# Kernel optimization log

Hardware: AMD Instinct MI355X
Metric: run time of the kernel (lower is better)

## Reference

```python
import math
import jax, jax.numpy as jnp
import numpy as np

B, T, C = 4, 2048, 1024
H = 16
HS = C // H  # head_size = 64

def setup_inputs() -> dict:
    key = jax.random.key(0)
    k1, k2, k3 = jax.random.split(key, 3)
    x = jax.random.normal(k1, (B, T, C), dtype=jnp.float32)
    W_qkv = jax.random.normal(k2, (C, 3 * C), dtype=jnp.float32) * (1.0 / math.sqrt(C))
    W_proj = jax.random.normal(k3, (C, C), dtype=jnp.float32) * (1.0 / math.sqrt(C))
    b_proj = jnp.zeros((C,), dtype=jnp.float32)
    return {"x": x, "W_qkv": W_qkv, "W_proj": W_proj, "b_proj": b_proj}

def reference(x, W_qkv, W_proj, b_proj):
    Bx, Tx, Cx = x.shape
    qkv = x @ W_qkv  # [B,T,3C]
    q, k, v = jnp.split(qkv, 3, axis=-1)
    # [B,T,C] -> [B,H,T,HS]
    def heads(t):
        return t.reshape(Bx, Tx, H, HS).transpose(0, 2, 1, 3)
    q, k, v = heads(q), heads(k), heads(v)
    scores = jnp.einsum('bhqd,bhkd->bhqk', q, k) / math.sqrt(HS)
    causal = jnp.tril(jnp.ones((Tx, Tx), dtype=bool))
    scores = jnp.where(causal, scores, -jnp.inf)
    attn = jax.nn.softmax(scores, axis=-1)
    out = jnp.einsum('bhqk,bhkd->bhqd', attn, v)  # [B,H,T,HS]
    out = out.transpose(0, 2, 1, 3).reshape(Bx, Tx, Cx)
    return out @ W_proj + b_proj
```

## Files before the change

kernel.cpp:

```cpp
#include <hip/hip_runtime.h>
#include <hip/hip_bf16.h>
#include <cstdint>
#include <cstddef>

using bf16 = __hip_bfloat16;
typedef __attribute__((ext_vector_type(8))) short short8;
typedef __attribute__((ext_vector_type(4))) float floatx4;

#define B_ 4
#define T_ 2048
#define C_ 1024
#define H_ 16
#define HS_ 64
#define BT_ (B_*T_)
#define N3C (3*C_)

#define MFMA16(a,b,c) __builtin_amdgcn_mfma_f32_16x16x32_bf16((a),(b),(c),0,0,0)

#if __has_builtin(__builtin_amdgcn_exp2f)
#define EXP2(x) __builtin_amdgcn_exp2f(x)
#else
#define EXP2(x) exp2f(x)
#endif

static __device__ __forceinline__ void gld16(const bf16* g, bf16* l) {
  __builtin_amdgcn_global_load_lds(
      (const __attribute__((address_space(1))) unsigned int*)g,
      (__attribute__((address_space(3))) unsigned int*)l, 16, 0, 0);
}

__global__ void k_cast(const float* __restrict__ in, bf16* __restrict__ out, int n4) {
  int i = blockIdx.x * blockDim.x + threadIdx.x;
  if (i >= n4) return;
  float4 v = ((const float4*)in)[i];
  union { bf16 b[4]; uint2 u; } cvt;
  cvt.b[0] = __float2bfloat16(v.x);
  cvt.b[1] = __float2bfloat16(v.y);
  cvt.b[2] = __float2bfloat16(v.z);
  cvt.b[3] = __float2bfloat16(v.w);
  ((uint2*)out)[i] = cvt.u;
}

__global__ void k_tcast(const float* __restrict__ in, bf16* __restrict__ out, int K, int N) {
  __shared__ float tile[64][65];
  const int k0 = blockIdx.y * 64, n0 = blockIdx.x * 64;
  const int tid = threadIdx.x;
  const int r = tid >> 6, c = tid & 63;
  #pragma unroll
  for (int j = 0; j < 16; ++j)
    tile[r + j*4][c] = in[(size_t)(k0 + r + j*4) * N + n0 + c];
  __syncthreads();
  #pragma unroll
  for (int j = 0; j < 16; ++j) {
    int rr = r + j*4;
    out[(size_t)(n0 + rr) * K + k0 + c] = __float2bfloat16(tile[c][rr]);
  }
}

__global__ void k_vtrans(const bf16* __restrict__ Vb, bf16* __restrict__ Vt) {
  __shared__ unsigned short tile[64*65];
  const int tid = threadIdx.x;
  const int bh = blockIdx.y, t0 = blockIdx.x * 64;
  const unsigned int* src = (const unsigned int*)(Vb + (size_t)bh * T_ * HS_ + (size_t)t0 * HS_);
  #pragma unroll
  for (int it = 0; it < 8; ++it) {
    int id = it*256 + tid;
    int row = id >> 5, cd = id & 31;
    unsigned int v = src[row*32 + cd];
    tile[row*65 + cd*2]     = (unsigned short)(v & 0xffff);
    tile[row*65 + cd*2 + 1] = (unsigned short)(v >> 16);
  }
  __syncthreads();
  bf16* dst = Vt + (size_t)bh * HS_ * T_ + t0;
  #pragma unroll
  for (int it = 0; it < 8; ++it) {
    int o = it*256 + tid;
    int d = o >> 5, tp = o & 31;
    int k0p = tp + (tp & 16);
    unsigned int lo = tile[k0p*65 + d];
    unsigned int hi = tile[(k0p + 16)*65 + d];
    ((unsigned int*)(dst + (size_t)d * T_))[tp] = lo | (hi << 16);
  }
}

template<int MODE, int NB>
__global__ __launch_bounds__(256, 2)
void k_gemm(const bf16* __restrict__ A, const bf16* __restrict__ Bt,
            int N, int K,
            bf16* __restrict__ Qb, bf16* __restrict__ Kb, bf16* __restrict__ Vb,
            float* __restrict__ Out, const float* __restrict__ bias)
{
  __shared__ bf16 sA[2][128*32];
  __shared__ bf16 sB[2][128*32];
  const int tid  = threadIdx.x;
  const int lane = tid & 63, wave = tid >> 6;
  const int quad = lane >> 4, l16 = lane & 15;
  const int wm = wave >> 1, wn = wave & 1;

  const int g = blockIdx.x;
  const int xcd = g & 7;
  const int local = g >> 3;
  const int nb = local % NB;
  const int mb = (local / NB) * 8 + xcd;
  const int m0 = mb * 128, n0 = nb * 128;

  const int ra = tid >> 2;
  const int gc = (tid & 3) ^ ((ra >> 1) & 3);
  const bf16* aptr = A  + (size_t)(m0 + ra) * K + gc*8;
  const bf16* bptr = Bt + (size_t)(n0 + ra) * K + gc*8;
  const size_t rowjump = (size_t)64 * K;

  floatx4 acc[4][4] = {};
  const int KI = K >> 5;
  const int pc = quad ^ ((l16 >> 1) & 3);

  for (int i = 0; i <= KI; ++i) {
    __syncthreads();
    if (i < KI) {
      const int k0 = i << 5;
      bf16* sa = sA[i & 1]; bf16* sb = sB[i & 1];
      gld16(aptr + k0,           sa + tid*8);
      gld16(aptr + rowjump + k0, sa + 2048 + tid*8);
      gld16(bptr + k0,           sb + tid*8);
      gld16(bptr + rowjump + k0, sb + 2048 + tid*8);
    }
    if (i == 0) continue;
    const bf16* sa = sA[(i-1) & 1];
    const bf16* sb = sB[(i-1) & 1];
    short8 af[4], bfm[4];
    #pragma unroll
    for (int ii = 0; ii < 4; ++ii)
      af[ii] = *(const short8*)&sa[(wm*64 + ii*16 + l16) * 32 + pc*8];
    #pragma unroll
    for (int ii = 0; ii < 4; ++ii)
      bfm[ii] = *(const short8*)&sb[(wn*64 + ii*16 + l16) * 32 + pc*8];
    #pragma unroll
    for (int ii = 0; ii < 4; ++ii)
      #pragma unroll
      for (int j = 0; j < 4; ++j)
        acc[ii][j] = MFMA16(af[ii], bfm[j], acc[ii][j]);
  }

  #pragma unroll
  for (int i = 0; i < 4; ++i) {
    const int rowb = m0 + wm*64 + i*16 + quad*4;
    #pragma unroll
    for (int j = 0; j < 4; ++j) {
      const int col = n0 + wn*64 + j*16 + l16;
      #pragma unroll
      for (int r = 0; r < 4; ++r) {
        const float v = acc[i][j][r];
        const int rr = rowb + r;
        if (MODE == 0) {
          const int b = rr >> 11, t = rr & 2047;
          const int h = (col >> 6) & 15, d = col & 63;
          const size_t addr = (((size_t)(b*H_ + h) * T_ + t) << 6) + d;
          if (col < C_) {
            Qb[addr] = __float2bfloat16(v * 0.18033688f);
          } else if (col < 2*C_) {
            Kb[addr] = __float2bfloat16(v);
          } else {
            Vb[addr] = __float2bfloat16(v);
          }
        } else {
          Out[(size_t)rr * N + col] = v + bias[col];
        }
      }
    }
  }
}

__global__ __launch_bounds__(256, 2)
void k_attn(const bf16* __restrict__ Q, const bf16* __restrict__ K,
            const bf16* __restrict__ Vt, bf16* __restrict__ att)
{
  __shared__ bf16 kbuf[2][64*64];
  __shared__ bf16 vbuf[2][64*64];
  __shared__ bf16 pbuf[4][32*64];

  const int tid  = threadIdx.x;
  const int lane = tid & 63, wave = tid >> 6;
  const int quad = lane >> 4, l16 = lane & 15;
  const int x7 = l16 & 7;

  const int g  = blockIdx.x;
  const int bh = (g & 7) * 8 + (g >> 6);
  const int bx = (g >> 3) & 7;
  const int b = bh >> 4, h = bh & 15;

  const bf16* Qp = Q  + (size_t)bh * T_ * HS_;
  const bf16* Kp = K  + (size_t)bh * T_ * HS_;
  const bf16* Vp = Vt + (size_t)bh * HS_ * T_;

  const int qbase[2] = { (15-bx)*128 + wave*32, bx*128 + wave*32 };
  const int ntk0 = 32 - 2*bx;
  const int ntk1 = 2*bx + 2;

  short8 qf[2][2][2];
  #pragma unroll
  for (int t = 0; t < 2; ++t)
    #pragma unroll
    for (int mt = 0; mt < 2; ++mt)
      #pragma unroll
      for (int ss = 0; ss < 2; ++ss)
        qf[t][mt][ss] = *(const short8*)(Qp + (size_t)(qbase[t] + mt*16 + l16) * HS_ + ss*32 + quad*8);

  floatx4 o[2][2][4] = {};
  float lrow[2][2][4] = {};

  const bf16* kg[2]; const bf16* vg[2];
  int ldsoff[2];
  #pragma unroll
  for (int it = 0; it < 2; ++it) {
    const int c = it*256 + tid;
    const int row = c >> 3;
    const int col = (c & 7) ^ (row & 7);
    kg[it] = Kp + (size_t)row * HS_ + col*8;
    vg[it] = Vp + (size_t)row * T_ + col*8;
    ldsoff[it] = c*8;
  }

  bf16* pw = pbuf[wave];
  unsigned int* pw32 = (unsigned int*)pw;
  const int c0 = l16 >> 2;
  const int dwl = l16 & 3;

  for (int i = 0; i <= ntk0; ++i) {
    __syncthreads();
    if (i < ntk0) {
      const int stk0 = i * 64;
      bf16* kb = kbuf[i & 1];
      bf16* vb = vbuf[i & 1];
      #pragma unroll
      for (int it = 0; it < 2; ++it) {
        gld16(kg[it] + (size_t)stk0 * HS_, kb + ldsoff[it]);
        gld16(vg[it] + stk0,               vb + ldsoff[it]);
      }
    }
    if (i == 0) continue;
    const int tk  = i - 1;
    const int tk0 = tk * 64;
    const bf16* kb = kbuf[tk & 1];
    const bf16* vb = vbuf[tk & 1];

    #pragma unroll
    for (int t = 0; t < 2; ++t) {
      if (t == 1 && tk >= ntk1) break;
      if (tk0 > qbase[t] + 31) continue;

      floatx4 s[2][4] = {};
      #pragma unroll
      for (int nt = 0; nt < 4; ++nt) {
        const int key = nt*16 + l16;
        #pragma unroll
        for (int ss = 0; ss < 2; ++ss) {
          short8 kf = *(const short8*)&kb[(key*8 + ((ss*4+quad) ^ x7))*8];
          s[0][nt] = MFMA16(qf[t][0][ss], kf, s[0][nt]);
          s[1][nt] = MFMA16(qf[t][1][ss], kf, s[1][nt]);
        }
      }

      if (tk0 + 63 > qbase[t]) {
        #pragma unroll
        for (int mt = 0; mt < 2; ++mt)
          #pragma unroll
          for (int nt = 0; nt < 4; ++nt) {
            const int key = tk0 + nt*16 + l16;
            #pragma unroll
            for (int r = 0; r < 4; ++r) {
              const int qr = qbase[t] + mt*16 + quad*4 + r;
              if (key > qr) s[mt][nt][r] = -1e30f;
            }
          }
      }

      #pragma unroll
      for (int mt = 0; mt < 2; ++mt) {
        #pragma unroll
        for (int r = 0; r < 4; ++r) {
          const float p0 = EXP2(s[mt][0][r]), p1 = EXP2(s[mt][1][r]);
          const float p2 = EXP2(s[mt][2][r]), p3 = EXP2(s[mt][3][r]);
          lrow[t][mt][r] += (p0 + p1) + (p2 + p3);
          const int q = mt*16 + quad*4 + r;
          const unsigned w0 = __builtin_amdgcn_perm(__float_as_uint(p1), __float_as_uint(p0), 0x07060302u);
          const unsigned w1 = __builtin_amdgcn_perm(__float_as_uint(p3), __float_as_uint(p2), 0x07060302u);
          pw32[q*32 + (((c0 + q)     & 7) << 2) + dwl] = w0;
          pw32[q*32 + (((c0 + q + 4) & 7) << 2) + dwl] = w1;
        }
      }

      #pragma unroll
      for (int ss = 0; ss < 2; ++ss) {
        short8 pf0 = *(const short8*)&pw[l16*64      + ((4*ss + quad + l16) & 7)*8];
        short8 pf1 = *(const short8*)&pw[(16+l16)*64 + ((4*ss + quad + l16) & 7)*8];
        #pragma unroll
        for (int nd = 0; nd < 4; ++nd) {
          const int d = nd*16 + l16;
          short8 vf = *(const short8*)&vb[(d*8 + ((ss*4+quad) ^ x7))*8];
          o[t][0][nd] = MFMA16(pf0, vf, o[t][0][nd]);
          o[t][1][nd] = MFMA16(pf1, vf, o[t][1][nd]);
        }
      }
    }
  }

  #pragma unroll
  for (int t = 0; t < 2; ++t) {
    #pragma unroll
    for (int mt = 0; mt < 2; ++mt) {
      #pragma unroll
      for (int r = 0; r < 4; ++r) {
        float lsum = lrow[t][mt][r];
        lsum += __shfl_xor(lsum, 1);
        lsum += __shfl_xor(lsum, 2);
        lsum += __shfl_xor(lsum, 4);
        lsum += __shfl_xor(lsum, 8);
        const float inv = 1.0f / lsum;
        const int tt = qbase[t] + mt*16 + quad*4 + r;
        #pragma unroll
        for (int nd = 0; nd < 4; ++nd)
          att[(size_t)(b*T_ + tt) * C_ + h*64 + nd*16 + l16] =
              __float2bfloat16(o[t][mt][nd][r] * inv);
      }
    }
  }
}

extern "C" void kernel_launch(void* const* d_in, const int* in_sizes, int n_in,
                              void* d_out, int out_size, void* d_ws, size_t ws_size,
                              hipStream_t stream) {
  const float* x     = (const float*)d_in[0];
  const float* Wqkv  = (const float*)d_in[1];
  const float* Wproj = (const float*)d_in[2];
  const float* bproj = (const float*)d_in[3];
  float* out = (float*)d_out;

  char* ws = (char*)d_ws;
  bf16* xb     = (bf16*)(ws + 0);
  bf16* wqkvT  = (bf16*)(ws + 16777216);
  bf16* wprojT = (bf16*)(ws + 23068672);
  bf16* Qb     = (bf16*)(ws + 25165824);
  bf16* Kb     = (bf16*)(ws + 41943040);
  bf16* Vt     = (bf16*)(ws + 58720256);
  bf16* att    = (bf16*)(ws + 75497472);
  bf16* Vb     = att;

  k_cast<<<dim3(BT_*C_/4/256), 256, 0, stream>>>(x, xb, BT_*C_/4);
  k_tcast<<<dim3(N3C/64, C_/64), 256, 0, stream>>>(Wqkv, wqkvT, C_, N3C);
  k_tcast<<<dim3(C_/64, C_/64), 256, 0, stream>>>(Wproj, wprojT, C_, C_);
  k_gemm<0, 24><<<dim3(1536), 256, 0, stream>>>(
      xb, wqkvT, N3C, C_, Qb, Kb, Vb, nullptr, nullptr);
  k_vtrans<<<dim3(T_/64, B_*H_), 256, 0, stream>>>(Vb, Vt);
  k_attn<<<dim3(512), 256, 0, stream>>>(Qb, Kb, Vt, att);
  k_gemm<1, 8><<<dim3(512), 256, 0, stream>>>(
      att, wprojT, C_, C_, nullptr, nullptr, nullptr, out, bproj);
}
```

Baseline: 253.9 us.

## Fuse V transpose into QKV GEMM epilogue and merge cast kernels

The three input-cast kernels become a single prep launch, which saves launch overhead. The separate V transpose kernel is removed. Instead, blocks in the QKV GEMM that produce V columns stage the tile in shared memory and write V directly in the transposed, permuted layout that attention expects. This avoids one full write and read of the V tensor and one kernel launch. The cost is a bigger shared-memory footprint, about 33 KB, plus an extra barrier and LDS staging in those GEMM blocks.

```diff
diff --git a/kernel.cpp b/kernel.cpp
--- a/kernel.cpp
+++ b/kernel.cpp
@@ -29,22 +29,41 @@
       (__attribute__((address_space(3))) unsigned int*)l, 16, 0, 0);
 }
 
-__global__ void k_cast(const float* __restrict__ in, bf16* __restrict__ out, int n4) {
-  int i = blockIdx.x * blockDim.x + threadIdx.x;
-  if (i >= n4) return;
-  float4 v = ((const float4*)in)[i];
-  union { bf16 b[4]; uint2 u; } cvt;
-  cvt.b[0] = __float2bfloat16(v.x);
-  cvt.b[1] = __float2bfloat16(v.y);
-  cvt.b[2] = __float2bfloat16(v.z);
-  cvt.b[3] = __float2bfloat16(v.w);
-  ((uint2*)out)[i] = cvt.u;
-}
-
-__global__ void k_tcast(const float* __restrict__ in, bf16* __restrict__ out, int K, int N) {
+static __device__ __forceinline__ unsigned short f2bf_us(float x) {
+  bf16 b = __float2bfloat16(x);
+  return *(unsigned short*)&b;
+}
+
+__global__ __launch_bounds__(256)
+void k_prep(const float* __restrict__ x, bf16* __restrict__ xb,
+            const float* __restrict__ Wqkv, bf16* __restrict__ wqkvT,
+            const float* __restrict__ Wproj, bf16* __restrict__ wprojT)
+{
+  const int bid = blockIdx.x, tid = threadIdx.x;
   __shared__ float tile[64][65];
-  const int k0 = blockIdx.y * 64, n0 = blockIdx.x * 64;
-  const int tid = threadIdx.x;
+
+  if (bid < 8192) {
+    const int i = bid*256 + tid;
+    float4 v = ((const float4*)x)[i];
+    union { bf16 b[4]; uint2 u; } cvt;
+    cvt.b[0] = __float2bfloat16(v.x);
+    cvt.b[1] = __float2bfloat16(v.y);
+    cvt.b[2] = __float2bfloat16(v.z);
+    cvt.b[3] = __float2bfloat16(v.w);
+    ((uint2*)xb)[i] = cvt.u;
+    return;
+  }
+
+  const float* in; bf16* out; int N, n0, k0;
+  if (bid < 8960) {
+    const int j = bid - 8192;
+    in = Wqkv; out = wqkvT; N = N3C;
+    n0 = (j % 48) * 64; k0 = (j / 48) * 64;
+  } else {
+    const int j = bid - 8960;
+    in = Wproj; out = wprojT; N = C_;
+    n0 = (j % 16) * 64; k0 = (j / 16) * 64;
+  }
   const int r = tid >> 6, c = tid & 63;
   #pragma unroll
   for (int j = 0; j < 16; ++j)
@@ -53,33 +72,7 @@
   #pragma unroll
   for (int j = 0; j < 16; ++j) {
     int rr = r + j*4;
-    out[(size_t)(n0 + rr) * K + k0 + c] = __float2bfloat16(tile[c][rr]);
-  }
-}
-
-__global__ void k_vtrans(const bf16* __restrict__ Vb, bf16* __restrict__ Vt) {
-  __shared__ unsigned short tile[64*65];
-  const int tid = threadIdx.x;
-  const int bh = blockIdx.y, t0 = blockIdx.x * 64;
-  const unsigned int* src = (const unsigned int*)(Vb + (size_t)bh * T_ * HS_ + (size_t)t0 * HS_);
-  #pragma unroll
-  for (int it = 0; it < 8; ++it) {
-    int id = it*256 + tid;
-    int row = id >> 5, cd = id & 31;
-    unsigned int v = src[row*32 + cd];
-    tile[row*65 + cd*2]     = (unsigned short)(v & 0xffff);
-    tile[row*65 + cd*2 + 1] = (unsigned short)(v >> 16);
-  }
-  __syncthreads();
-  bf16* dst = Vt + (size_t)bh * HS_ * T_ + t0;
-  #pragma unroll
-  for (int it = 0; it < 8; ++it) {
-    int o = it*256 + tid;
-    int d = o >> 5, tp = o & 31;
-    int k0p = tp + (tp & 16);
-    unsigned int lo = tile[k0p*65 + d];
-    unsigned int hi = tile[(k0p + 16)*65 + d];
-    ((unsigned int*)(dst + (size_t)d * T_))[tp] = lo | (hi << 16);
+    out[(size_t)(n0 + rr) * C_ + k0 + c] = __float2bfloat16(tile[c][rr]);
   }
 }
 
@@ -87,11 +80,13 @@
 __global__ __launch_bounds__(256, 2)
 void k_gemm(const bf16* __restrict__ A, const bf16* __restrict__ Bt,
             int N, int K,
-            bf16* __restrict__ Qb, bf16* __restrict__ Kb, bf16* __restrict__ Vb,
+            bf16* __restrict__ Qb, bf16* __restrict__ Kb, bf16* __restrict__ Vt,
             float* __restrict__ Out, const float* __restrict__ bias)
 {
-  __shared__ bf16 sA[2][128*32];
-  __shared__ bf16 sB[2][128*32];
+  __shared__ __align__(16) char smem[33856];
+  bf16* const sAb = (bf16*)smem;
+  bf16* const sBb = (bf16*)(smem + 16384);
+
   const int tid  = threadIdx.x;
   const int lane = tid & 63, wave = tid >> 6;
   const int quad = lane >> 4, l16 = lane & 15;
@@ -118,15 +113,16 @@
     __syncthreads();
     if (i < KI) {
       const int k0 = i << 5;
-      bf16* sa = sA[i & 1]; bf16* sb = sB[i & 1];
+      bf16* sa = sAb + (i & 1) * 4096;
+      bf16* sb = sBb + (i & 1) * 4096;
       gld16(aptr + k0,           sa + tid*8);
       gld16(aptr + rowjump + k0, sa + 2048 + tid*8);
       gld16(bptr + k0,           sb + tid*8);
       gld16(bptr + rowjump + k0, sb + 2048 + tid*8);
     }
     if (i == 0) continue;
-    const bf16* sa = sA[(i-1) & 1];
-    const bf16* sb = sB[(i-1) & 1];
+    const bf16* sa = sAb + ((i-1) & 1) * 4096;
+    const bf16* sb = sBb + ((i-1) & 1) * 4096;
     short8 af[4], bfm[4];
     #pragma unroll
     for (int ii = 0; ii < 4; ++ii)
@@ -141,29 +137,61 @@
         acc[ii][j] = MFMA16(af[ii], bfm[j], acc[ii][j]);
   }
 
-  #pragma unroll
-  for (int i = 0; i < 4; ++i) {
-    const int rowb = m0 + wm*64 + i*16 + quad*4;
-    #pragma unroll
-    for (int j = 0; j < 4; ++j) {
-      const int col = n0 + wn*64 + j*16 + l16;
-      #pragma unroll
-      for (int r = 0; r < 4; ++r) {
-        const float v = acc[i][j][r];
-        const int rr = rowb + r;
-        if (MODE == 0) {
-          const int b = rr >> 11, t = rr & 2047;
-          const int h = (col >> 6) & 15, d = col & 63;
-          const size_t addr = (((size_t)(b*H_ + h) * T_ + t) << 6) + d;
-          if (col < C_) {
-            Qb[addr] = __float2bfloat16(v * 0.18033688f);
-          } else if (col < 2*C_) {
-            Kb[addr] = __float2bfloat16(v);
+  if (MODE == 0 && nb >= 16) {
+    __syncthreads();
+    unsigned short* epi = (unsigned short*)smem;
+    #pragma unroll
+    for (int i = 0; i < 4; ++i) {
+      const int tl = wm*64 + i*16 + quad*4;
+      #pragma unroll
+      for (int j = 0; j < 4; ++j) {
+        const int ccl = wn*64 + j*16 + l16;
+        #pragma unroll
+        for (int r = 0; r < 4; ++r)
+          epi[ccl*132 + tl + r] = f2bf_us(acc[i][j][r]);
+      }
+    }
+    __syncthreads();
+    const int b  = m0 >> 11;
+    const int t0 = m0 & 2047;
+    const int h0 = (n0 - 2*C_) >> 6;
+    #pragma unroll
+    for (int it = 0; it < 32; ++it) {
+      const int id = it*256 + tid;
+      const int tp = id & 31;
+      const int rest = id >> 5;
+      const int tl64 = (rest & 1) * 64;
+      const int ccl = rest >> 1;
+      const int k0p = tp + (tp & 16);
+      const unsigned lo = epi[ccl*132 + tl64 + k0p];
+      const unsigned hi = epi[ccl*132 + tl64 + k0p + 16];
+      const int h = h0 + (ccl >> 6), d = ccl & 63;
+      unsigned* row = (unsigned*)(Vt + ((size_t)(b*H_ + h) * HS_ + d) * T_);
+      row[(t0 >> 1) + tl64/2 + tp] = lo | (hi << 16);
+    }
+  } else {
+    #pragma unroll
+    for (int i = 0; i < 4; ++i) {
+      const int rowb = m0 + wm*64 + i*16 + quad*4;
+      #pragma unroll
+      for (int j = 0; j < 4; ++j) {
+        const int col = n0 + wn*64 + j*16 + l16;
+        #pragma unroll
+        for (int r = 0; r < 4; ++r) {
+          const float v = acc[i][j][r];
+          const int rr = rowb + r;
+          if (MODE == 0) {
+            const int b = rr >> 11, t = rr & 2047;
+            const int h = (col >> 6) & 15, d = col & 63;
+            const size_t addr = (((size_t)(b*H_ + h) * T_ + t) << 6) + d;
+            if (nb < 8) {
+              Qb[addr] = __float2bfloat16(v * 0.18033688f);
+            } else {
+              Kb[addr] = __float2bfloat16(v);
+            }
           } else {
-            Vb[addr] = __float2bfloat16(v);
+            Out[(size_t)rr * N + col] = v + bias[col];
           }
-        } else {
-          Out[(size_t)rr * N + col] = v + bias[col];
         }
       }
     }
@@ -343,14 +371,10 @@
   bf16* Kb     = (bf16*)(ws + 41943040);
   bf16* Vt     = (bf16*)(ws + 58720256);
   bf16* att    = (bf16*)(ws + 75497472);
-  bf16* Vb     = att;
-
-  k_cast<<<dim3(BT_*C_/4/256), 256, 0, stream>>>(x, xb, BT_*C_/4);
-  k_tcast<<<dim3(N3C/64, C_/64), 256, 0, stream>>>(Wqkv, wqkvT, C_, N3C);
-  k_tcast<<<dim3(C_/64, C_/64), 256, 0, stream>>>(Wproj, wprojT, C_, C_);
+
+  k_prep<<<dim3(9216), 256, 0, stream>>>(x, xb, Wqkv, wqkvT, Wproj, wprojT);
   k_gemm<0, 24><<<dim3(1536), 256, 0, stream>>>(
-      xb, wqkvT, N3C, C_, Qb, Kb, Vb, nullptr, nullptr);
-  k_vtrans<<<dim3(T_/64, B_*H_), 256, 0, stream>>>(Vb, Vt);
+      xb, wqkvT, N3C, C_, Qb, Kb, Vt, nullptr, nullptr);
   k_attn<<<dim3(512), 256, 0, stream>>>(Qb, Kb, Vt, att);
   k_gemm<1, 8><<<dim3(512), 256, 0, stream>>>(
       att, wprojT, C_, C_, nullptr, nullptr, nullptr, out, bproj);
```

Result: faster. 237.6 us (-6.4%).
